# Performance work log

Measured on AMD Instinct MI355X. Metric: run time of the kernel, lower is better.

## Reference

```python
import jax, jax.numpy as jnp
import numpy as np

PATCH_SIZE = 128
IMG = 256


def _circle_perimeter(r_o, c_o, radius):
    # skimage.draw.circle_perimeter, method='bresenham' (midpoint circle),
    # including the duplicate octant-boundary points that skimage emits.
    rr, cc = [], []
    c, r = 0, radius
    d = 3 - 2 * radius
    while c <= r:
        rr += [r, -r, r, -r, c, -c, c, -c]
        cc += [c, c, -c, -c, r, r, -r, -r]
        if d < 0:
            d += 4 * c + 6
        else:
            d += 4 * (c - r) + 10
            r -= 1
        c += 1
    return np.asarray(rr) + r_o, np.asarray(cc) + c_o


def _radial_indices(patch_size, img):
    cy, cx = img // 2, img // 2
    rr_all, cc_all, seg_all = [], [], []
    for radius in range(1, patch_size - 1):  # radii 1..patch_size-2
        rr, cc = _circle_perimeter(cy, cx, radius)
        rr_all.append(rr)
        cc_all.append(cc)
        seg_all.append(np.full(rr.shape[0], radius - 1))
    return (np.concatenate(rr_all).astype(np.int32),
            np.concatenate(cc_all).astype(np.int32),
            np.concatenate(seg_all).astype(np.int32))


def setup_inputs() -> dict:
    key = jax.random.key(0)
    k1, k2 = jax.random.split(key)
    inp = jax.random.normal(k1, (64, 3, IMG, IMG), dtype=jnp.float32)
    tgt = jax.random.normal(k2, (64, 3, IMG, IMG), dtype=jnp.float32)
    w = np.float32(np.arange(0, 1, 1 / (PATCH_SIZE - 1)))  # length 127
    weights = jnp.asarray(w / np.sum(w))
    rr_idx, cc_idx, seg_ids = _radial_indices(PATCH_SIZE, IMG)
    return {"input": inp, "target": tgt, "weights": weights,
            "rr_idx": jnp.asarray(rr_idx), "cc_idx": jnp.asarray(cc_idx),
            "seg_ids": jnp.asarray(seg_ids)}


def reference(input, target, weights, rr_idx, cc_idx, seg_ids):
    B, C = input.shape[0], input.shape[1]
    R = weights.shape[0]          # patch_size - 1 curve bins
    nseg = R - 1                  # radii 1..patch_size-2
    f1 = jnp.fft.fft2(input)      # complex64 [B,C,H,W]
    f2 = jnp.fft.fft2(target)
    p1 = f1[:, :, rr_idx, cc_idx]  # [B,C,Ntot]
    p2 = f2[:, :, rr_idx, cc_idx]
    # original sums num/den over ALL dims (batch+channel+perimeter points)
    cross = jnp.sum(p1 * jnp.conj(p2), axis=(0, 1))        # [Ntot] complex
    pw1 = jnp.sum(jnp.abs(p1) ** 2, axis=(0, 1))           # [Ntot]
    pw2 = jnp.sum(jnp.abs(p2) ** 2, axis=(0, 1))
    num = jnp.abs(jax.ops.segment_sum(cross, seg_ids, num_segments=nseg))
    den = (jax.ops.segment_sum(pw1, seg_ids, num_segments=nseg) *
           jax.ops.segment_sum(pw2, seg_ids, num_segments=nseg))
    curve = jnp.concatenate([jnp.ones((1,), jnp.float32),
                             (num / jnp.sqrt(den)).astype(jnp.float32)])  # [R]
    # curve is identical across (b, c); Linear(R,1,bias=False) then total sum
    curve_full = jnp.broadcast_to(curve, (B, C, R))
    return jnp.sum(curve_full @ weights)
```

## Files before the change

### kernel.cpp

```cpp
#include <hip/hip_runtime.h>
#include <math.h>

#define NSEG 126

__device__ __forceinline__ unsigned bitrev8(unsigned v) { return __brev(v) >> 24; }

__device__ __forceinline__ void fft256(float2 x[4], int lane) {
    const float PI = 3.14159265358979323846f;
    {
        float s, c;
        __sincosf(-PI * (float)lane * (1.0f / 128.0f), &s, &c);
        float2 w0 = make_float2(c, s);
        float2 w1 = make_float2(s, -c);
        float2 u, t, d;
        u = x[0]; t = x[2];
        x[0] = make_float2(u.x + t.x, u.y + t.y);
        d = make_float2(u.x - t.x, u.y - t.y);
        x[2] = make_float2(d.x * w0.x - d.y * w0.y, d.x * w0.y + d.y * w0.x);
        u = x[1]; t = x[3];
        x[1] = make_float2(u.x + t.x, u.y + t.y);
        d = make_float2(u.x - t.x, u.y - t.y);
        x[3] = make_float2(d.x * w1.x - d.y * w1.y, d.x * w1.y + d.y * w1.x);
    }
    {
        float s, c;
        __sincosf(-PI * (float)lane * (1.0f / 64.0f), &s, &c);
        float2 w = make_float2(c, s);
        float2 u, t, d;
        u = x[0]; t = x[1];
        x[0] = make_float2(u.x + t.x, u.y + t.y);
        d = make_float2(u.x - t.x, u.y - t.y);
        x[1] = make_float2(d.x * w.x - d.y * w.y, d.x * w.y + d.y * w.x);
        u = x[2]; t = x[3];
        x[2] = make_float2(u.x + t.x, u.y + t.y);
        d = make_float2(u.x - t.x, u.y - t.y);
        x[3] = make_float2(d.x * w.x - d.y * w.y, d.x * w.y + d.y * w.x);
    }
    #pragma unroll
    for (int hbit = 5; hbit >= 0; hbit--) {
        int h = 1 << hbit;
        int j = lane & (h - 1);
        float s, c;
        __sincosf(-PI * (float)j / (float)h, &s, &c);
        bool up = (lane & h) != 0;
        #pragma unroll
        for (int i = 0; i < 4; i++) {
            float px = __shfl_xor(x[i].x, h);
            float py = __shfl_xor(x[i].y, h);
            if (up) {
                float dx = px - x[i].x, dy = py - x[i].y;
                x[i] = make_float2(dx * c - dy * s, dx * s + dy * c);
            } else {
                x[i] = make_float2(x[i].x + px, x[i].y + py);
            }
        }
    }
}

__global__ void prep_zero(float* acc, int* counts) {
    int i = blockIdx.x * 256 + threadIdx.x;
    if (i < NSEG * 3) acc[i] = 0.f;
    if (i < 128) counts[i] = 0;
}

__device__ __forceinline__ bool keep_point(int r, int c) {
    return (c > 128) || (c == 128 && r > 128);
}

__global__ void prep_hist(const int* __restrict__ rr, const int* __restrict__ cc,
                          int n, int* counts) {
    int i = blockIdx.x * 256 + threadIdx.x;
    if (i < n) {
        int c = cc[i], r = rr[i];
        if (keep_point(r, c)) {
            int j = (int)(bitrev8((unsigned)c) >> 1);
            atomicAdd(&counts[j], 1);
        }
    }
}

__global__ void prep_scan(const int* __restrict__ counts, int* starts, int* cursor) {
    int lane = threadIdx.x;
    int2 c = reinterpret_cast<const int2*>(counts)[lane];
    int lsum = c.x + c.y;
    int pre = lsum;
    #pragma unroll
    for (int off = 1; off < 64; off <<= 1) {
        int v = __shfl_up(pre, off);
        if (lane >= off) pre += v;
    }
    int excl = pre - lsum;
    int2 outv = make_int2(excl, excl + c.x);
    reinterpret_cast<int2*>(starts)[lane] = outv;
    reinterpret_cast<int2*>(cursor)[lane] = outv;
    if (lane == 63) starts[128] = excl + c.x + c.y;
}

__global__ void prep_scatter(const int* __restrict__ rr, const int* __restrict__ cc,
                             const int* __restrict__ seg, int n, int* cursor,
                             int* b_pos, int* b_seg) {
    int i = blockIdx.x * 256 + threadIdx.x;
    if (i < n) {
        int c = cc[i], r = rr[i];
        if (keep_point(r, c)) {
            int j = (int)(bitrev8((unsigned)c) >> 1);
            int pos = atomicAdd(&cursor[j], 1);
            b_pos[pos] = (int)bitrev8((unsigned)r);
            b_seg[pos] = seg[i];
        }
    }
}

__global__ __launch_bounds__(1024) void rowfft_kernel(
    const float* __restrict__ inp, const float* __restrict__ tgt,
    float2* __restrict__ G, int pair_base)
{
    int bid  = blockIdx.x;
    int limg = bid >> 4;
    int wv   = threadIdx.x >> 6;
    int lane = threadIdx.x & 63;
    int row  = ((bid & 15) << 4) + wv;
    int t    = limg & 1;
    int p    = pair_base + (limg >> 1);
    const float* src = (t == 0 ? inp : tgt) + (((size_t)p) << 16) + ((size_t)row << 8);

    float2 x[4];
    #pragma unroll
    for (int i = 0; i < 4; i++) x[i] = make_float2(src[i * 64 + lane], 0.f);

    fft256(x, lane);

    float2* dst = G + (((size_t)limg) << 15) + ((size_t)row << 7);
    if (lane & 1) {
        #pragma unroll
        for (int i = 0; i < 4; i++) dst[i * 32 + (lane >> 1)] = x[i];
    }
}

#define TP 17
__global__ __launch_bounds__(1024) void colfft_gather_kernel(
    const float2* __restrict__ G, const int* __restrict__ starts,
    const int* __restrict__ b_pos, const int* __restrict__ b_seg,
    float* __restrict__ acc)
{
    __shared__ float2 tile[2 * 256 * TP];
    __shared__ float accl[NSEG * 3];
    int tid  = threadIdx.x;
    int wv   = tid >> 6;
    int lane = tid & 63;
    int plocal = blockIdx.x >> 3;
    int cg     = blockIdx.x & 7;
    int j0     = cg << 4;

    for (int i = tid; i < NSEG * 3; i += 1024) accl[i] = 0.f;

    const float2* Gp = G + (((size_t)plocal) << 16);

    #pragma unroll
    for (int k = 0; k < 8; k++) {
        int idx = tid + (k << 10);
        int img = idx >> 12;
        int x   = (idx >> 4) & 255;
        int c   = idx & 15;
        tile[img * (256 * TP) + x * TP + c] =
            Gp[((size_t)img << 15) + (x << 7) + j0 + c];
    }
    __syncthreads();

    float2 x1[4], x2[4];
    #pragma unroll
    for (int i = 0; i < 4; i++) {
        int xx = i * 64 + lane;
        x1[i] = tile[xx * TP + wv];
        x2[i] = tile[256 * TP + xx * TP + wv];
    }
    __syncthreads();

    fft256(x1, lane);
    fft256(x2, lane);

    float2* F1 = tile + wv * 512;
    float2* F2 = F1 + 256;
    #pragma unroll
    for (int i = 0; i < 4; i++) {
        F1[i * 64 + lane] = x1[i];
        F2[i * 64 + lane] = x2[i];
    }
    __syncthreads();

    int col = j0 + wv;
    int s0 = starts[col], s1 = starts[col + 1];
    for (int e = s0 + lane; e < s1; e += 64) {
        int pos = b_pos[e];
        int sg  = b_seg[e];
        float2 f1 = F1[pos];
        float2 f2 = F2[pos];
        atomicAdd(&accl[sg * 3 + 0], f1.x * f2.x + f1.y * f2.y);
        atomicAdd(&accl[sg * 3 + 1], f1.x * f1.x + f1.y * f1.y);
        atomicAdd(&accl[sg * 3 + 2], f2.x * f2.x + f2.y * f2.y);
    }
    __syncthreads();

    for (int i = tid; i < NSEG * 3; i += 1024) {
        float v = accl[i];
        if (v != 0.f) atomicAdd(&acc[i], v);
    }
}

__global__ void final_kernel(const float* __restrict__ acc, const float* __restrict__ w,
                             float* __restrict__ out, float scale) {
    int lane = threadIdx.x;
    float val = 0.f;
    for (int s = lane; s < NSEG; s += 64) {
        float cr = acc[s * 3 + 0];
        float p1 = acc[s * 3 + 1];
        float p2 = acc[s * 3 + 2];
        float den = p1 * p2;
        float curve = den > 0.f ? fabsf(cr) * rsqrtf(den) : 0.f;
        val += curve * w[s + 1];
    }
    if (lane == 0) val += w[0];
    #pragma unroll
    for (int off = 32; off > 0; off >>= 1) val += __shfl_down(val, off);
    if (lane == 0) out[0] = scale * val;
}

extern "C" void kernel_launch(void* const* d_in, const int* in_sizes, int n_in,
                              void* d_out, int out_size, void* d_ws, size_t ws_size,
                              hipStream_t stream)
{
    const float* inp = (const float*)d_in[0];
    const float* tgt = (const float*)d_in[1];
    const float* wts = (const float*)d_in[2];
    const int*   rr  = (const int*)d_in[3];
    const int*   cc  = (const int*)d_in[4];
    const int*   sg  = (const int*)d_in[5];
    int npts   = in_sizes[3];
    int npairs = in_sizes[0] >> 16;

    char* ws = (char*)d_ws;
    float* acc    = (float*)(ws + 0);
    int*   counts = (int*)(ws + 2048);
    int*   starts = (int*)(ws + 2560);
    int*   cursor = (int*)(ws + 3584);
    int*   b_pos  = (int*)(ws + 4096);
    int*   b_seg  = b_pos + npts;
    size_t goff = 4096 + (size_t)2 * npts * 4;
    goff = (goff + 255) & ~(size_t)255;
    float2* G = (float2*)(ws + goff);

    size_t per_pair = (size_t)2 * 256 * 128 * sizeof(float2);
    int maxchunk = (int)((ws_size > goff ? (ws_size - goff) : 0) / per_pair);
    if (maxchunk < 1) maxchunk = 1;
    if (maxchunk > npairs) maxchunk = npairs;

    prep_zero<<<2, 256, 0, stream>>>(acc, counts);
    prep_hist<<<(npts + 255) / 256, 256, 0, stream>>>(rr, cc, npts, counts);
    prep_scan<<<1, 64, 0, stream>>>(counts, starts, cursor);
    prep_scatter<<<(npts + 255) / 256, 256, 0, stream>>>(rr, cc, sg, npts, cursor, b_pos, b_seg);

    for (int pb = 0; pb < npairs; pb += maxchunk) {
        int cp = npairs - pb < maxchunk ? npairs - pb : maxchunk;
        rowfft_kernel<<<cp * 32, 1024, 0, stream>>>(inp, tgt, G, pb);
        colfft_gather_kernel<<<cp * 8, 1024, 0, stream>>>(G, starts, b_pos, b_seg, acc);
    }

    final_kernel<<<1, 64, 0, stream>>>(acc, wts, (float*)d_out, (float)npairs);
}
```

Before: 285.8 us.

## Pack input and target into one complex FFT and transpose row output

Input and target rows are loaded as the real and imaginary parts of a single complex signal, which halves the row FFT work. The two spectra are then recovered at the gather step through the conjugate-symmetric split F(k) and F(N-k). The row FFT now writes a transposed layout through a shared-memory tile, so each column FFT reads contiguously. Gather indices are packed into one int carrying the position, the mirrored position and the segment, which cuts index traffic. The cost is extra bit-reversal index logic and a more complex recovery formula whose correctness depends on the mirrored-column mapping.

```diff
diff --git a/kernel.cpp b/kernel.cpp
--- a/kernel.cpp
+++ b/kernel.cpp
@@ -58,7 +58,7 @@
 }
 
 __global__ void prep_zero(float* acc, int* counts) {
-    int i = blockIdx.x * 256 + threadIdx.x;
+    int i = threadIdx.x;
     if (i < NSEG * 3) acc[i] = 0.f;
     if (i < 128) counts[i] = 0;
 }
@@ -72,10 +72,7 @@
     int i = blockIdx.x * 256 + threadIdx.x;
     if (i < n) {
         int c = cc[i], r = rr[i];
-        if (keep_point(r, c)) {
-            int j = (int)(bitrev8((unsigned)c) >> 1);
-            atomicAdd(&counts[j], 1);
-        }
+        if (keep_point(r, c)) atomicAdd(&counts[255 - c], 1);
     }
 }
 
@@ -98,15 +95,16 @@
 
 __global__ void prep_scatter(const int* __restrict__ rr, const int* __restrict__ cc,
                              const int* __restrict__ seg, int n, int* cursor,
-                             int* b_pos, int* b_seg) {
+                             int* b_pack) {
     int i = blockIdx.x * 256 + threadIdx.x;
     if (i < n) {
         int c = cc[i], r = rr[i];
         if (keep_point(r, c)) {
-            int j = (int)(bitrev8((unsigned)c) >> 1);
+            int j = 255 - c;
             int pos = atomicAdd(&cursor[j], 1);
-            b_pos[pos] = (int)bitrev8((unsigned)r);
-            b_seg[pos] = seg[i];
+            int pr = (int)bitrev8((unsigned)r);
+            int pm = (int)bitrev8((unsigned)(256 - r) & 255);
+            b_pack[pos] = pr | (pm << 8) | (seg[i] << 16);
         }
     }
 }
@@ -115,95 +113,89 @@
     const float* __restrict__ inp, const float* __restrict__ tgt,
     float2* __restrict__ G, int pair_base)
 {
-    int bid  = blockIdx.x;
-    int limg = bid >> 4;
-    int wv   = threadIdx.x >> 6;
-    int lane = threadIdx.x & 63;
-    int row  = ((bid & 15) << 4) + wv;
-    int t    = limg & 1;
-    int p    = pair_base + (limg >> 1);
-    const float* src = (t == 0 ? inp : tgt) + (((size_t)p) << 16) + ((size_t)row << 8);
+    __shared__ float2 T[256 * 17];
+    int bid    = blockIdx.x;
+    int plocal = bid >> 4;
+    int rowgrp = bid & 15;
+    int wv     = threadIdx.x >> 6;
+    int lane   = threadIdx.x & 63;
+    int row    = (rowgrp << 4) + wv;
+    size_t base = (((size_t)(pair_base + plocal)) << 16) + ((size_t)row << 8);
+    const float* s1 = inp + base;
+    const float* s2 = tgt + base;
 
     float2 x[4];
     #pragma unroll
-    for (int i = 0; i < 4; i++) x[i] = make_float2(src[i * 64 + lane], 0.f);
-
+    for (int i = 0; i < 4; i++) {
+        int e = i * 64 + lane;
+        x[i] = make_float2(s1[e], s2[e]);
+    }
     fft256(x, lane);
 
-    float2* dst = G + (((size_t)limg) << 15) + ((size_t)row << 7);
-    if (lane & 1) {
-        #pragma unroll
-        for (int i = 0; i < 4; i++) dst[i * 32 + (lane >> 1)] = x[i];
-    }
-}
-
-#define TP 17
-__global__ __launch_bounds__(1024) void colfft_gather_kernel(
+    #pragma unroll
+    for (int i = 0; i < 4; i++) T[(i * 64 + lane) * 17 + wv] = x[i];
+    __syncthreads();
+
+    float2* dst = G + (((size_t)plocal) << 16) + (rowgrp << 4);
+    int xl = threadIdx.x & 15;
+    int qb = threadIdx.x >> 4;
+    #pragma unroll
+    for (int ii = 0; ii < 4; ii++) {
+        int q = qb + (ii << 6);
+        dst[q * 256 + xl] = T[q * 17 + xl];
+    }
+}
+
+__global__ __launch_bounds__(512) void colfft_gather_kernel(
     const float2* __restrict__ G, const int* __restrict__ starts,
-    const int* __restrict__ b_pos, const int* __restrict__ b_seg,
-    float* __restrict__ acc)
+    const int* __restrict__ b_pack, float* __restrict__ acc)
 {
-    __shared__ float2 tile[2 * 256 * TP];
+    __shared__ float2 Fb[8 * 256];
     __shared__ float accl[NSEG * 3];
-    int tid  = threadIdx.x;
-    int wv   = tid >> 6;
-    int lane = tid & 63;
-    int plocal = blockIdx.x >> 3;
-    int cg     = blockIdx.x & 7;
-    int j0     = cg << 4;
-
-    for (int i = tid; i < NSEG * 3; i += 1024) accl[i] = 0.f;
-
-    const float2* Gp = G + (((size_t)plocal) << 16);
-
-    #pragma unroll
-    for (int k = 0; k < 8; k++) {
-        int idx = tid + (k << 10);
-        int img = idx >> 12;
-        int x   = (idx >> 4) & 255;
-        int c   = idx & 15;
-        tile[img * (256 * TP) + x * TP + c] =
-            Gp[((size_t)img << 15) + (x << 7) + j0 + c];
-    }
+    int tid    = threadIdx.x;
+    int wv     = tid >> 6;
+    int lane   = tid & 63;
+    int plocal = blockIdx.x >> 5;
+    int b      = blockIdx.x & 31;
+    int kp     = wv & 3;
+    int j      = (b << 2) + kp;
+    int v      = (wv < 4) ? (j + 1) : (255 - j);
+    int q      = (int)bitrev8((unsigned)v);
+
+    for (int i = tid; i < NSEG * 3; i += 512) accl[i] = 0.f;
+
+    const float2* col = G + (((size_t)plocal) << 16) + ((size_t)q << 8);
+    float2 x[4];
+    #pragma unroll
+    for (int i = 0; i < 4; i++) x[i] = col[i * 64 + lane];
+
+    fft256(x, lane);
+
+    float2* F = Fb + (wv << 8);
+    #pragma unroll
+    for (int i = 0; i < 4; i++) F[i * 64 + lane] = x[i];
     __syncthreads();
 
-    float2 x1[4], x2[4];
-    #pragma unroll
-    for (int i = 0; i < 4; i++) {
-        int xx = i * 64 + lane;
-        x1[i] = tile[xx * TP + wv];
-        x2[i] = tile[256 * TP + xx * TP + wv];
+    const float2* F_lo = Fb + (kp << 8);
+    const float2* F_hi = Fb + ((4 + kp) << 8);
+    int s0 = starts[j] + ((wv < 4) ? 0 : 64);
+    int s1 = starts[j + 1];
+    for (int e = s0 + lane; e < s1; e += 128) {
+        int pk = b_pack[e];
+        float2 a = F_hi[pk & 255];
+        float2 m = F_lo[(pk >> 8) & 255];
+        int sg = pk >> 16;
+        float f1x = a.x + m.x, f1y = a.y - m.y;
+        float dx  = a.x - m.x, dy  = a.y + m.y;
+        atomicAdd(&accl[sg * 3 + 0], f1x * dy - f1y * dx);
+        atomicAdd(&accl[sg * 3 + 1], f1x * f1x + f1y * f1y);
+        atomicAdd(&accl[sg * 3 + 2], dx * dx + dy * dy);
     }
     __syncthreads();
 
-    fft256(x1, lane);
-    fft256(x2, lane);
-
-    float2* F1 = tile + wv * 512;
-    float2* F2 = F1 + 256;
-    #pragma unroll
-    for (int i = 0; i < 4; i++) {
-        F1[i * 64 + lane] = x1[i];
-        F2[i * 64 + lane] = x2[i];
-    }
-    __syncthreads();
-
-    int col = j0 + wv;
-    int s0 = starts[col], s1 = starts[col + 1];
-    for (int e = s0 + lane; e < s1; e += 64) {
-        int pos = b_pos[e];
-        int sg  = b_seg[e];
-        float2 f1 = F1[pos];
-        float2 f2 = F2[pos];
-        atomicAdd(&accl[sg * 3 + 0], f1.x * f2.x + f1.y * f2.y);
-        atomicAdd(&accl[sg * 3 + 1], f1.x * f1.x + f1.y * f1.y);
-        atomicAdd(&accl[sg * 3 + 2], f2.x * f2.x + f2.y * f2.y);
-    }
-    __syncthreads();
-
-    for (int i = tid; i < NSEG * 3; i += 1024) {
-        float v = accl[i];
-        if (v != 0.f) atomicAdd(&acc[i], v);
+    for (int i = tid; i < NSEG * 3; i += 512) {
+        float s = accl[i];
+        if (s != 0.f) atomicAdd(&acc[i], s);
     }
 }
 
@@ -243,26 +235,25 @@
     int*   counts = (int*)(ws + 2048);
     int*   starts = (int*)(ws + 2560);
     int*   cursor = (int*)(ws + 3584);
-    int*   b_pos  = (int*)(ws + 4096);
-    int*   b_seg  = b_pos + npts;
-    size_t goff = 4096 + (size_t)2 * npts * 4;
+    int*   b_pack = (int*)(ws + 4096);
+    size_t goff = 4096 + (size_t)npts * 4;
     goff = (goff + 255) & ~(size_t)255;
     float2* G = (float2*)(ws + goff);
 
-    size_t per_pair = (size_t)2 * 256 * 128 * sizeof(float2);
+    size_t per_pair = (size_t)256 * 256 * sizeof(float2);
     int maxchunk = (int)((ws_size > goff ? (ws_size - goff) : 0) / per_pair);
     if (maxchunk < 1) maxchunk = 1;
     if (maxchunk > npairs) maxchunk = npairs;
 
-    prep_zero<<<2, 256, 0, stream>>>(acc, counts);
+    prep_zero<<<1, 512, 0, stream>>>(acc, counts);
     prep_hist<<<(npts + 255) / 256, 256, 0, stream>>>(rr, cc, npts, counts);
     prep_scan<<<1, 64, 0, stream>>>(counts, starts, cursor);
-    prep_scatter<<<(npts + 255) / 256, 256, 0, stream>>>(rr, cc, sg, npts, cursor, b_pos, b_seg);
+    prep_scatter<<<(npts + 255) / 256, 256, 0, stream>>>(rr, cc, sg, npts, cursor, b_pack);
 
     for (int pb = 0; pb < npairs; pb += maxchunk) {
         int cp = npairs - pb < maxchunk ? npairs - pb : maxchunk;
-        rowfft_kernel<<<cp * 32, 1024, 0, stream>>>(inp, tgt, G, pb);
-        colfft_gather_kernel<<<cp * 8, 1024, 0, stream>>>(G, starts, b_pos, b_seg, acc);
+        rowfft_kernel<<<cp * 16, 1024, 0, stream>>>(inp, tgt, G, pb);
+        colfft_gather_kernel<<<cp * 32, 512, 0, stream>>>(G, starts, b_pack, acc);
     }
 
     final_kernel<<<1, 64, 0, stream>>>(acc, wts, (float*)d_out, (float)npairs);
```

New measurement: 323.6 us. +13.2%, slower.
